# Kernel tuning notes

Measured on AMD Instinct MI355X. Metric: run time of the kernel, lower is better.

Reference implementation:

```python
import jax, jax.numpy as jnp
import numpy as np

IN_DIM = 512
HEADS = 8
HEAD_DIM = IN_DIM // HEADS
SCALE = HEAD_DIM ** -0.5


def setup_inputs() -> dict:
    key = jax.random.key(0)
    ks = jax.random.split(key, 9)
    B, C, H, W = 16, IN_DIM, 32, 32
    std = 1.0 / np.sqrt(C)  # ~ conv2d default init scale
    inp = {
        "x": jax.random.normal(ks[0], (B, C, H, W), dtype=jnp.float32),
        "wq": jax.random.normal(ks[1], (C, C), dtype=jnp.float32) * std,
        "bq": jax.random.normal(ks[2], (C,), dtype=jnp.float32) * std,
        "wk": jax.random.normal(ks[3], (C, C), dtype=jnp.float32) * std,
        "bk": jax.random.normal(ks[4], (C,), dtype=jnp.float32) * std,
        "wv": jax.random.normal(ks[5], (C, C), dtype=jnp.float32) * std,
        "bv": jax.random.normal(ks[6], (C,), dtype=jnp.float32) * std,
        "wo": jax.random.normal(ks[7], (C, C), dtype=jnp.float32) * std,
        "bo": jax.random.normal(ks[8], (C,), dtype=jnp.float32) * std,
        "gamma": jnp.zeros((1,), dtype=jnp.float32) + 0.1,  # learned residual scale
    }
    return inp


def reference(x, wq, bq, wk, bk, wv, bv, wo, bo, gamma):
    B, C, H, W = x.shape
    N = H * W
    hd = HEAD_DIM
    # flatten spatial: [B, C, N]
    xf = x.reshape(B, C, N)
    # 1x1 convs == channel matmuls: [B, C, N]
    q = jnp.einsum('oc,bcn->bon', wq, xf) + bq[None, :, None]
    k = jnp.einsum('oc,bcn->bon', wk, xf) + bk[None, :, None]
    v = jnp.einsum('oc,bcn->bon', wv, xf) + bv[None, :, None]
    # split heads: [B, heads, head_dim, N]
    q = q.reshape(B, HEADS, hd, N)
    k = k.reshape(B, HEADS, hd, N)
    v = v.reshape(B, HEADS, hd, N)
    # energy[b,h,i,j] = sum_d q[b,h,d,i] * k[b,h,d,j]
    energy = jnp.einsum('bhdi,bhdj->bhij', q, k) * SCALE
    attn = jax.nn.softmax(energy, axis=-1)  # [B, heads, N, N]
    # out[b,h,d,i] = sum_j attn[b,h,i,j] * v[b,h,d,j]
    out = jnp.einsum('bhij,bhdj->bhdi', attn, v)
    out = out.reshape(B, C, N)
    out = jnp.einsum('oc,bcn->bon', wo, out) + bo[None, :, None]
    y = gamma[0] * out.reshape(B, C, H, W) + x
    return y
```

## Files before the change

### kernel.cpp

```cpp
#include <hip/hip_runtime.h>
#include <hip/hip_bf16.h>

#define BB 16
#define CC 512
#define HH 8
#define DD 64
#define NN 1024

using f32x4  = __attribute__((ext_vector_type(4))) float;
typedef __bf16 bf16x8 __attribute__((ext_vector_type(8)));
typedef __bf16 bf16x4 __attribute__((ext_vector_type(4)));

#define MFMA16(a, b, c) __builtin_amdgcn_mfma_f32_16x16x32_bf16((a), (b), (c), 0, 0, 0)

#define WAITVM8 asm volatile("s_waitcnt vmcnt(8)" ::: "memory")
#define WAITVM4 asm volatile("s_waitcnt vmcnt(4)" ::: "memory")
#define WAITVM0 asm volatile("s_waitcnt vmcnt(0)" ::: "memory")
#define BARRIER __builtin_amdgcn_s_barrier()
#define SCHEDB  __builtin_amdgcn_sched_barrier(0)

__device__ __forceinline__ void glds16(const __hip_bfloat16* g, __hip_bfloat16* l) {
  typedef __attribute__((address_space(1))) const void gv_t;
  typedef __attribute__((address_space(3))) void lv_t;
  __builtin_amdgcn_global_load_lds((gv_t*)g, (lv_t*)l, 16, 0, 0);
}

__global__ __launch_bounds__(256) void k_prep(
    const float* __restrict__ x, __hip_bfloat16* __restrict__ xT,
    __hip_bfloat16* __restrict__ xbf,
    const float* __restrict__ wq, const float* __restrict__ wk,
    const float* __restrict__ wv, const float* __restrict__ wo,
    __hip_bfloat16* __restrict__ wqb) {
  __shared__ float tile[64][65];
  const int L = blockIdx.x;
  const int t = threadIdx.x;
  if (L >= 2048) {
    const int j = L - 2048;
    const int mat = j >> 8;
    const float* s = (mat == 0) ? wq : (mat == 1) ? wk : (mat == 2) ? wv : wo;
    __hip_bfloat16* o = wqb + (size_t)mat * CC * CC;
    const int i = ((j & 255) * 256 + t) * 4;
    float4 v = *(const float4*)(s + i);
    alignas(8) __hip_bfloat16 tm[4];
    tm[0] = __float2bfloat16(v.x);
    tm[1] = __float2bfloat16(v.y);
    tm[2] = __float2bfloat16(v.z);
    tm[3] = __float2bfloat16(v.w);
    *(bf16x4*)(o + i) = *(const bf16x4*)tm;
    return;
  }
  const int c = L & 7, r = L >> 3;
  const int b  = c * 2 + (r >> 7);
  const int rr = r & 127;
  const int bn = (rr & 15) * 64;
  const int bc = (rr >> 4) * 64;

  const float* xb = x + ((size_t)b * CC + bc) * NN + bn;
  __hip_bfloat16* xbo = xbf + ((size_t)b * CC + bc) * NN + bn;
  const int r0 = t >> 4;
  const int c0 = (t & 15) * 4;
  for (int p = 0; p < 4; ++p) {
    const int rw = r0 + p * 16;
    float4 v = *(const float4*)(xb + (size_t)rw * NN + c0);
    tile[rw][c0 + 0] = v.x;
    tile[rw][c0 + 1] = v.y;
    tile[rw][c0 + 2] = v.z;
    tile[rw][c0 + 3] = v.w;
    alignas(8) __hip_bfloat16 tm[4];
    tm[0] = __float2bfloat16(v.x);
    tm[1] = __float2bfloat16(v.y);
    tm[2] = __float2bfloat16(v.z);
    tm[3] = __float2bfloat16(v.w);
    *(bf16x4*)(xbo + (size_t)rw * NN + c0) = *(const bf16x4*)tm;
  }
  __syncthreads();

  __hip_bfloat16* xo = xT + ((size_t)b * NN + bn) * CC + bc;
  const int rn0 = t >> 3;
  const int cc0 = (t & 7) * 8;
  for (int p = 0; p < 2; ++p) {
    const int rn = rn0 + p * 32;
    alignas(16) __hip_bfloat16 tmp[8];
    for (int j = 0; j < 8; ++j) tmp[j] = __float2bfloat16(tile[cc0 + j][rn]);
    *(bf16x8*)(xo + (size_t)rn * CC + cc0) = *(const bf16x8*)tmp;
  }
}

__global__ __launch_bounds__(256, 2) void k_gemm_qkv(
    const __hip_bfloat16* __restrict__ Wqkv,
    const __hip_bfloat16* __restrict__ Xt,
    const float* __restrict__ bq, const float* __restrict__ bk,
    const float* __restrict__ bv,
    __hip_bfloat16* __restrict__ qT, __hip_bfloat16* __restrict__ kT,
    __hip_bfloat16* __restrict__ vO, float qscale) {
  __shared__ __hip_bfloat16 Wl[2][8192];
  __shared__ __hip_bfloat16 Xl[2][8192];
  const int b  = blockIdx.z;
  const int ot = blockIdx.y * 128;
  const int nt = blockIdx.x * 128;
  const int sector = blockIdx.y >> 2;
  const int t  = threadIdx.x;
  const int w  = t >> 6, l = t & 63;
  const int wr = w >> 1, wc = w & 1;
  const int lg = l >> 4, lr16 = l & 15;

  f32x4 acc[4][4] = {};

  const __hip_bfloat16* Wp = Wqkv + (size_t)ot * CC;
  const __hip_bfloat16* Xp = Xt + ((size_t)b * NN + nt) * CC;
  const int srow = w * 8 + (l >> 3);
  const int scol = ((l & 7) ^ ((l >> 3) & 7)) * 8;
  const __hip_bfloat16* wsrc = Wp + (size_t)srow * CC + scol;
  const __hip_bfloat16* xsrc = Xp + (size_t)srow * CC + scol;

  auto STAGE = [&](int bn, int k0) {
#pragma unroll
    for (int i = 0; i < 4; ++i)
      glds16(wsrc + (size_t)(i * 32) * CC + k0, &Wl[bn][(w * 8 + i * 32) * 64]);
#pragma unroll
    for (int i = 0; i < 4; ++i)
      glds16(xsrc + (size_t)(i * 32) * CC + k0, &Xl[bn][(w * 8 + i * 32) * 64]);
  };

  const int s7 = lr16 & 7;
  const int slot0 = ((lg) ^ s7) * 8;
  const int slot1 = ((4 + lg) ^ s7) * 8;
  const int rowA = (wr * 64 + lr16) * 64;
  const int rowB = (wc * 64 + lr16) * 64;

  auto STEP = [&](int bn) {
    const __hip_bfloat16* Wb = &Wl[bn][0];
    const __hip_bfloat16* Xb = &Xl[bn][0];
#pragma unroll
    for (int ks = 0; ks < 2; ++ks) {
      const int sl = ks ? slot1 : slot0;
      bf16x8 af[4], bfr[4];
#pragma unroll
      for (int mi = 0; mi < 4; ++mi) af[mi] = *(const bf16x8*)(Wb + rowA + mi * 1024 + sl);
#pragma unroll
      for (int nj = 0; nj < 4; ++nj) bfr[nj] = *(const bf16x8*)(Xb + rowB + nj * 1024 + sl);
      __builtin_amdgcn_s_setprio(1);
#pragma unroll
      for (int mi = 0; mi < 4; ++mi)
#pragma unroll
        for (int nj = 0; nj < 4; ++nj)
          acc[mi][nj] = MFMA16(af[mi], bfr[nj], acc[mi][nj]);
      __builtin_amdgcn_s_setprio(0);
    }
  };

  STAGE(0, 0);
  STAGE(1, 64);
  for (int kt = 0; kt < 7; ++kt) {
    WAITVM8;
    BARRIER; SCHEDB;
    STEP(kt & 1);
    BARRIER;
    if (kt < 6) STAGE(kt & 1, (kt + 2) * 64);
  }
  WAITVM0; BARRIER; SCHEDB; STEP(1);

  const float* bias = (sector == 0) ? bq : (sector == 1) ? bk : bv;
  const float scale = (sector == 0) ? qscale : 1.0f;
  __hip_bfloat16* outT = (sector == 0) ? qT : kT;

  for (int mi = 0; mi < 4; ++mi) {
    const int og = ot + wr * 64 + mi * 16 + lg * 4;
    const int o0 = og & 511;
    for (int nj = 0; nj < 4; ++nj) {
      const int n = nt + wc * 64 + nj * 16 + lr16;
      if (sector < 2) {
        alignas(8) __hip_bfloat16 tmp[4];
        for (int rj = 0; rj < 4; ++rj)
          tmp[rj] = __float2bfloat16((acc[mi][nj][rj] + bias[o0 + rj]) * scale);
        const int hh = o0 >> 6, d0 = o0 & 63;
        *(bf16x4*)(outT + (((size_t)(b * HH + hh)) * NN + n) * DD + d0) = *(const bf16x4*)tmp;
      } else {
        for (int rj = 0; rj < 4; ++rj)
          vO[((size_t)b * CC + o0 + rj) * NN + n] =
              __float2bfloat16(acc[mi][nj][rj] + bias[o0 + rj]);
      }
    }
  }
}

__global__ __launch_bounds__(256, 4) void k_gemm_o(
    const __hip_bfloat16* __restrict__ W,
    const __hip_bfloat16* __restrict__ Xt,
    const float* __restrict__ bias,
    const __hip_bfloat16* __restrict__ xbf,
    const float* __restrict__ gamma,
    float* __restrict__ y) {
  __shared__ __hip_bfloat16 Wl[2][4096];
  __shared__ __hip_bfloat16 Xl[2][4096];
  const int b  = blockIdx.z;
  const int ot = blockIdx.y * 128;
  const int nt = blockIdx.x * 128;
  const int t  = threadIdx.x;
  const int w  = t >> 6, l = t & 63;
  const int wr = w >> 1, wc = w & 1;
  const int lg = l >> 4, lr16 = l & 15;

  f32x4 acc[4][4] = {};

  const int srow = w * 16 + (l >> 2);
  const int scol = ((l & 3) ^ ((l >> 3) & 3)) * 8;
  const __hip_bfloat16* ws0 = W + (size_t)(ot + srow) * CC + scol;
  const __hip_bfloat16* xs0 = Xt + ((size_t)b * NN + nt + srow) * CC + scol;

  const int sx  = (lg ^ ((lr16 >> 1) & 3)) * 8;
  const int rdA = (wr * 64 + lr16) * 32 + sx;
  const int rdB = (wc * 64 + lr16) * 32 + sx;

#define STAGEO(bn, k0)                                        \
  do {                                                        \
    glds16(ws0 + (k0), &Wl[bn][w * 512]);                     \
    glds16(ws0 + (size_t)64 * CC + (k0), &Wl[bn][2048 + w * 512]); \
    glds16(xs0 + (k0), &Xl[bn][w * 512]);                     \
    glds16(xs0 + (size_t)64 * CC + (k0), &Xl[bn][2048 + w * 512]); \
  } while (0)

  STAGEO(0, 0);
  for (int kt = 0; kt < 16; ++kt) {
    WAITVM0;
    BARRIER; SCHEDB;
    if (kt < 15) STAGEO((kt + 1) & 1, (kt + 1) * 32);
    const __hip_bfloat16* Wb = &Wl[kt & 1][0];
    const __hip_bfloat16* Xb = &Xl[kt & 1][0];
    bf16x8 af[4], bfr[4];
#pragma unroll
    for (int mi = 0; mi < 4; ++mi) af[mi] = *(const bf16x8*)(Wb + rdA + mi * 512);
#pragma unroll
    for (int nj = 0; nj < 4; ++nj) bfr[nj] = *(const bf16x8*)(Xb + rdB + nj * 512);
    __builtin_amdgcn_s_setprio(1);
#pragma unroll
    for (int mi = 0; mi < 4; ++mi)
#pragma unroll
      for (int nj = 0; nj < 4; ++nj)
        acc[mi][nj] = MFMA16(af[mi], bfr[nj], acc[mi][nj]);
    __builtin_amdgcn_s_setprio(0);
  }
#undef STAGEO

  const float g = gamma[0];
  for (int mi = 0; mi < 4; ++mi) {
    const int o0 = ot + wr * 64 + mi * 16 + lg * 4;
    for (int nj = 0; nj < 4; ++nj) {
      const int n = nt + wc * 64 + nj * 16 + lr16;
      for (int rj = 0; rj < 4; ++rj) {
        const size_t idx = ((size_t)b * CC + o0 + rj) * NN + n;
        y[idx] = g * (acc[mi][nj][rj] + bias[o0 + rj]) + __bfloat162float(xbf[idx]);
      }
    }
  }
}

__global__ __launch_bounds__(256, 2) void k_attn(
    const __hip_bfloat16* __restrict__ qT,
    const __hip_bfloat16* __restrict__ kT,
    const __hip_bfloat16* __restrict__ v,
    __hip_bfloat16* __restrict__ attT) {
  __shared__ __hip_bfloat16 Kl[3][4096];
  __shared__ __hip_bfloat16 Vl[3][4096];

  const int L = blockIdx.x;
  const int c = L & 7, s = L >> 3;
  const int bh = c * 16 + (s >> 2);
  const int i0 = (s & 3) * 256;
  const int b = bh >> 3, h = bh & 7;
  const int t  = threadIdx.x;
  const int w  = t >> 6, l = t & 63;
  const int lg = l >> 4, lr = l & 15;

  const __hip_bfloat16* qb = qT + ((size_t)(b * HH + h)) * NN * DD;
  const __hip_bfloat16* kb = kT + ((size_t)(b * HH + h)) * NN * DD;
  const __hip_bfloat16* vb = v + ((size_t)b * CC + h * DD) * NN;

  bf16x8 qf[4][2];
#pragma unroll
  for (int g = 0; g < 4; ++g) {
    const __hip_bfloat16* qp = qb + (size_t)(i0 + w * 64 + g * 16 + lr) * DD + lg * 8;
    qf[g][0] = *(const bf16x8*)qp;
    qf[g][1] = *(const bf16x8*)(qp + 32);
  }

  const int rA = w * 8 + (l >> 3);
  const int rB = rA + 32;
  const int sA = (l & 7) ^ ((rA & 3) ^ (((rA >> 3) & 1) << 2));
  const __hip_bfloat16* gKA = kb + rA * DD + sA * 8;
  const __hip_bfloat16* gKB = kb + rB * DD + sA * 8;
  const __hip_bfloat16* gVA = vb + (size_t)rA * NN + sA * 8;
  const __hip_bfloat16* gVB = vb + (size_t)rB * NN + sA * 8;

  auto STAGE = [&](int bufn, int tile) {
    glds16(gKA + (size_t)tile * 4096, &Kl[bufn][w * 512]);
    glds16(gKB + (size_t)tile * 4096, &Kl[bufn][2048 + w * 512]);
    glds16(gVA + tile * 64, &Vl[bufn][w * 512]);
    glds16(gVB + tile * 64, &Vl[bufn][2048 + w * 512]);
  };

  const int swzK = (lr & 3) ^ (((lr >> 2) & 1) << 2);
  const int krl  = 8 * (lr >> 2) + (lr & 3);
  const int offK0 = krl * 64 + ((lg ^ swzK) * 8);
  const int offK1 = krl * 64 + (((lg + 4) ^ swzK) * 8);
  const int swzV = (lr & 3) ^ (((lr >> 3) & 1) << 2);

  f32x4 accO[4][4] = {};
  f32x4 accL[4] = {};
  const bf16x8 ones = {(__bf16)1.f, (__bf16)1.f, (__bf16)1.f, (__bf16)1.f,
                       (__bf16)1.f, (__bf16)1.f, (__bf16)1.f, (__bf16)1.f};

  STAGE(0, 0);
  STAGE(1, 1);
  STAGE(2, 2);

  for (int tile = 0; tile < 16; ++tile) {
    const int bufn = tile % 3;
    if (tile < 14) { WAITVM8; } else if (tile == 14) { WAITVM4; } else { WAITVM0; }
    BARRIER; SCHEDB;

    const __hip_bfloat16* Kb = &Kl[bufn][0];
    const __hip_bfloat16* Vb = &Vl[bufn][0];

    __builtin_amdgcn_s_setprio(1);
    f32x4 st[4][4];
#pragma unroll
    for (int jt = 0; jt < 4; ++jt) {
      const int jo = (jt >> 1) * 2048 + (jt & 1) * 256;
      bf16x8 kf0 = *(const bf16x8*)(Kb + jo + offK0);
      bf16x8 kf1 = *(const bf16x8*)(Kb + jo + offK1);
#pragma unroll
      for (int g = 0; g < 4; ++g) {
        f32x4 a = {};
        a = MFMA16(kf0, qf[g][0], a);
        a = MFMA16(kf1, qf[g][1], a);
        st[g][jt] = a;
      }
    }
    __builtin_amdgcn_s_setprio(0);

    bf16x8 pf[4][2];
#pragma unroll
    for (int g = 0; g < 4; ++g) {
      union { bf16x8 v8; __hip_bfloat16 h[8]; } pk0, pk1;
#pragma unroll
      for (int jt = 0; jt < 4; ++jt)
#pragma unroll
        for (int rj = 0; rj < 4; ++rj) {
          const float p = __builtin_amdgcn_exp2f(st[g][jt][rj]);
          if (jt < 2) pk0.h[(jt & 1) * 4 + rj] = __float2bfloat16(p);
          else        pk1.h[(jt & 1) * 4 + rj] = __float2bfloat16(p);
        }
      pf[g][0] = pk0.v8;
      pf[g][1] = pk1.v8;
    }

    __builtin_amdgcn_s_setprio(1);
#pragma unroll
    for (int ks = 0; ks < 2; ++ks) {
#pragma unroll
      for (int dt = 0; dt < 4; ++dt) {
        bf16x8 vf = *(const bf16x8*)(Vb + (dt * 16 + lr) * 64 + (((ks * 4 + lg) ^ swzV) * 8));
#pragma unroll
        for (int g = 0; g < 4; ++g)
          accO[g][dt] = MFMA16(pf[g][ks], vf, accO[g][dt]);
      }
#pragma unroll
      for (int g = 0; g < 4; ++g)
        accL[g] = MFMA16(pf[g][ks], ones, accL[g]);
    }
    __builtin_amdgcn_s_setprio(0);

    BARRIER;
    if (tile < 13) STAGE(bufn, tile + 3);
  }

#pragma unroll
  for (int g = 0; g < 4; ++g)
#pragma unroll
    for (int dt = 0; dt < 4; ++dt) {
      f32x4 o;
#pragma unroll
      for (int rj = 0; rj < 4; ++rj) o[rj] = accO[g][dt][rj] / accL[g][rj];
#pragma unroll
      for (int rj = 0; rj < 4; ++rj) {
        const int i = i0 + w * 64 + g * 16 + 4 * lg + rj;
        const int d = dt * 16 + lr;
        attT[((size_t)b * NN + i) * CC + h * DD + d] = __float2bfloat16(o[rj]);
      }
    }
}

extern "C" void kernel_launch(void* const* d_in, const int* in_sizes, int n_in,
                              void* d_out, int out_size, void* d_ws, size_t ws_size,
                              hipStream_t stream) {
  const float* x     = (const float*)d_in[0];
  const float* wq    = (const float*)d_in[1];
  const float* bq    = (const float*)d_in[2];
  const float* wk    = (const float*)d_in[3];
  const float* bk    = (const float*)d_in[4];
  const float* wv    = (const float*)d_in[5];
  const float* bv    = (const float*)d_in[6];
  const float* wo    = (const float*)d_in[7];
  const float* bo    = (const float*)d_in[8];
  const float* gamma = (const float*)d_in[9];
  float* y = (float*)d_out;

  char* ws = (char*)d_ws;
  const size_t szT = (size_t)BB * NN * CC * 2;
  __hip_bfloat16* xT  = (__hip_bfloat16*)(ws);
  __hip_bfloat16* qT  = (__hip_bfloat16*)(ws + szT);
  __hip_bfloat16* kTb = (__hip_bfloat16*)(ws + 2 * szT);
  __hip_bfloat16* vB  = (__hip_bfloat16*)(ws + 3 * szT);
  __hip_bfloat16* xbf = (__hip_bfloat16*)(ws + 4 * szT);
  __hip_bfloat16* wqb = (__hip_bfloat16*)(ws + 5 * szT);
  __hip_bfloat16* wob = wqb + (size_t)3 * CC * CC;

  k_prep<<<dim3(2048 + 1024), 256, 0, stream>>>(x, xT, xbf, wq, wk, wv, wo, wqb);

  const float qsc = 0.125f * 1.44269504f;
  k_gemm_qkv<<<dim3(NN / 128, 12, BB), 256, 0, stream>>>(
      wqb, xT, bq, bk, bv, qT, kTb, vB, qsc);

  k_attn<<<dim3(BB * HH * (NN / 256)), 256, 0, stream>>>(qT, kTb, vB, xT);

  k_gemm_o<<<dim3(NN / 128, CC / 128, BB), 256, 0, stream>>>(
      wob, xT, bo, xbf, gamma, y);
}
```

Baseline: 115.7 us.

## Enlarge QKV GEMM tiles to 256x256 with 8 waves and phased prefetch

The QKV projection GEMM now uses 256x256 output tiles with 512 threads (8 waves, each computing 128x64), and flattens batch and spatial into a single N dimension. The K loop is split into four phases per step that interleave the next A/B tile loads with MFMA work, double buffering A one step ahead and B two steps ahead. The goal is more data reuse per LDS load and better overlap of global-to-LDS copies with compute. The costs are 128KB of LDS per block, more accumulator registers, fewer blocks in flight, and extra barriers.

```diff
diff --git a/kernel.cpp b/kernel.cpp
--- a/kernel.cpp
+++ b/kernel.cpp
@@ -86,98 +86,123 @@
   }
 }
 
-__global__ __launch_bounds__(256, 2) void k_gemm_qkv(
+__global__ __launch_bounds__(512, 2) void k_gemm_qkv(
     const __hip_bfloat16* __restrict__ Wqkv,
     const __hip_bfloat16* __restrict__ Xt,
     const float* __restrict__ bq, const float* __restrict__ bk,
     const float* __restrict__ bv,
     __hip_bfloat16* __restrict__ qT, __hip_bfloat16* __restrict__ kT,
     __hip_bfloat16* __restrict__ vO, float qscale) {
-  __shared__ __hip_bfloat16 Wl[2][8192];
-  __shared__ __hip_bfloat16 Xl[2][8192];
-  const int b  = blockIdx.z;
-  const int ot = blockIdx.y * 128;
-  const int nt = blockIdx.x * 128;
-  const int sector = blockIdx.y >> 2;
-  const int t  = threadIdx.x;
-  const int w  = t >> 6, l = t & 63;
-  const int wr = w >> 1, wc = w & 1;
+  __shared__ __hip_bfloat16 Al[2][16384];
+  __shared__ __hip_bfloat16 Bl[2][16384];
+  const int ot = blockIdx.y * 256;
+  const int ng = blockIdx.x * 256;
+  const int sector = blockIdx.y >> 1;
+  const int t = threadIdx.x;
+  const int w = t >> 6, l = t & 63;
+  const int wr = w >> 2, wc = w & 3;
   const int lg = l >> 4, lr16 = l & 15;
 
-  f32x4 acc[4][4] = {};
+  f32x4 acc[8][4] = {};
+  bf16x8 bfr[4][2];
 
   const __hip_bfloat16* Wp = Wqkv + (size_t)ot * CC;
-  const __hip_bfloat16* Xp = Xt + ((size_t)b * NN + nt) * CC;
+  const __hip_bfloat16* Xp = Xt + (size_t)ng * CC;
   const int srow = w * 8 + (l >> 3);
   const int scol = ((l & 7) ^ ((l >> 3) & 7)) * 8;
-  const __hip_bfloat16* wsrc = Wp + (size_t)srow * CC + scol;
-  const __hip_bfloat16* xsrc = Xp + (size_t)srow * CC + scol;
-
-  auto STAGE = [&](int bn, int k0) {
-#pragma unroll
-    for (int i = 0; i < 4; ++i)
-      glds16(wsrc + (size_t)(i * 32) * CC + k0, &Wl[bn][(w * 8 + i * 32) * 64]);
-#pragma unroll
-    for (int i = 0; i < 4; ++i)
-      glds16(xsrc + (size_t)(i * 32) * CC + k0, &Xl[bn][(w * 8 + i * 32) * 64]);
+  const __hip_bfloat16* asrc = Wp + (size_t)srow * CC + scol;
+  const __hip_bfloat16* bsrc = Xp + (size_t)srow * CC + scol;
+
+  auto SA = [&](int buf, int kt, int h) {
+#pragma unroll
+    for (int i = 0; i < 2; ++i)
+      glds16(asrc + (size_t)(h * 128 + i * 64) * CC + kt * 64,
+             &Al[buf][(h * 128 + i * 64 + w * 8) * 64]);
   };
+  auto SB = [&](int buf, int kt, int h) {
+#pragma unroll
+    for (int i = 0; i < 2; ++i)
+      glds16(bsrc + (size_t)(h * 128 + i * 64) * CC + kt * 64,
+             &Bl[buf][(h * 128 + i * 64 + w * 8) * 64]);
+  };
 
   const int s7 = lr16 & 7;
-  const int slot0 = ((lg) ^ s7) * 8;
+  const int slot0 = (lg ^ s7) * 8;
   const int slot1 = ((4 + lg) ^ s7) * 8;
-  const int rowA = (wr * 64 + lr16) * 64;
+  const int rowA = (wr * 128 + lr16) * 64;
   const int rowB = (wc * 64 + lr16) * 64;
 
-  auto STEP = [&](int bn) {
-    const __hip_bfloat16* Wb = &Wl[bn][0];
-    const __hip_bfloat16* Xb = &Xl[bn][0];
-#pragma unroll
-    for (int ks = 0; ks < 2; ++ks) {
-      const int sl = ks ? slot1 : slot0;
-      bf16x8 af[4], bfr[4];
-#pragma unroll
-      for (int mi = 0; mi < 4; ++mi) af[mi] = *(const bf16x8*)(Wb + rowA + mi * 1024 + sl);
-#pragma unroll
-      for (int nj = 0; nj < 4; ++nj) bfr[nj] = *(const bf16x8*)(Xb + rowB + nj * 1024 + sl);
-      __builtin_amdgcn_s_setprio(1);
-#pragma unroll
-      for (int mi = 0; mi < 4; ++mi)
-#pragma unroll
-        for (int nj = 0; nj < 4; ++nj)
-          acc[mi][nj] = MFMA16(af[mi], bfr[nj], acc[mi][nj]);
-      __builtin_amdgcn_s_setprio(0);
-    }
-  };
-
-  STAGE(0, 0);
-  STAGE(1, 64);
-  for (int kt = 0; kt < 7; ++kt) {
-    WAITVM8;
-    BARRIER; SCHEDB;
-    STEP(kt & 1);
-    BARRIER;
-    if (kt < 6) STAGE(kt & 1, (kt + 2) * 64);
-  }
-  WAITVM0; BARRIER; SCHEDB; STEP(1);
+  SA(0, 0, 0); SA(0, 0, 1);
+  SB(0, 0, 0); SB(0, 0, 1);
+  SB(1, 1, 0); SB(1, 1, 1);
+  WAITVM4;
+  BARRIER;
+
+#define QPHASE(q, STG, WT)                                                  \
+  do {                                                                      \
+    bf16x8 a0 = *(const bf16x8*)(Ab + rowA + (2 * (q) + 0) * 1024 + slot0); \
+    bf16x8 a1 = *(const bf16x8*)(Ab + rowA + (2 * (q) + 0) * 1024 + slot1); \
+    bf16x8 a2 = *(const bf16x8*)(Ab + rowA + (2 * (q) + 1) * 1024 + slot0); \
+    bf16x8 a3 = *(const bf16x8*)(Ab + rowA + (2 * (q) + 1) * 1024 + slot1); \
+    STG;                                                                    \
+    WT;                                                                     \
+    BARRIER;                                                                \
+    asm volatile("s_waitcnt lgkmcnt(0)" ::: "memory");                      \
+    SCHEDB;                                                                 \
+    __builtin_amdgcn_s_setprio(1);                                          \
+    _Pragma("unroll")                                                       \
+    for (int nj = 0; nj < 4; ++nj) {                                        \
+      acc[2 * (q) + 0][nj] = MFMA16(a0, bfr[nj][0], acc[2 * (q) + 0][nj]);  \
+      acc[2 * (q) + 0][nj] = MFMA16(a1, bfr[nj][1], acc[2 * (q) + 0][nj]);  \
+      acc[2 * (q) + 1][nj] = MFMA16(a2, bfr[nj][0], acc[2 * (q) + 1][nj]);  \
+      acc[2 * (q) + 1][nj] = MFMA16(a3, bfr[nj][1], acc[2 * (q) + 1][nj]);  \
+    }                                                                       \
+    __builtin_amdgcn_s_setprio(0);                                          \
+    BARRIER;                                                                \
+  } while (0)
+
+  for (int j = 0; j < 8; ++j) {
+    const int p = j & 1, pn = p ^ 1;
+    const __hip_bfloat16* Ab = &Al[p][0];
+    const __hip_bfloat16* Bb = &Bl[p][0];
+#pragma unroll
+    for (int nj = 0; nj < 4; ++nj) {
+      bfr[nj][0] = *(const bf16x8*)(Bb + rowB + nj * 1024 + slot0);
+      bfr[nj][1] = *(const bf16x8*)(Bb + rowB + nj * 1024 + slot1);
+    }
+    QPHASE(0, if (j < 7) SA(pn, j + 1, 0), (void)0);
+    QPHASE(1, if (j < 7) SA(pn, j + 1, 1), (void)0);
+    QPHASE(2, if (j < 6) SB(p, j + 2, 0), (void)0);
+    QPHASE(3, if (j < 6) SB(p, j + 2, 1),
+           if (j < 6) { WAITVM4; } else { WAITVM0; });
+  }
+#undef QPHASE
 
   const float* bias = (sector == 0) ? bq : (sector == 1) ? bk : bv;
   const float scale = (sector == 0) ? qscale : 1.0f;
   __hip_bfloat16* outT = (sector == 0) ? qT : kT;
-
-  for (int mi = 0; mi < 4; ++mi) {
-    const int og = ot + wr * 64 + mi * 16 + lg * 4;
-    const int o0 = og & 511;
+  const int bb = ng >> 10;
+  const int nb = ng & 1023;
+  const int obase = (ot & 511) + wr * 128;
+
+#pragma unroll
+  for (int mi = 0; mi < 8; ++mi) {
+    const int o0 = obase + mi * 16 + lg * 4;
+#pragma unroll
     for (int nj = 0; nj < 4; ++nj) {
-      const int n = nt + wc * 64 + nj * 16 + lr16;
+      const int n = nb + wc * 64 + nj * 16 + lr16;
       if (sector < 2) {
         alignas(8) __hip_bfloat16 tmp[4];
+#pragma unroll
         for (int rj = 0; rj < 4; ++rj)
           tmp[rj] = __float2bfloat16((acc[mi][nj][rj] + bias[o0 + rj]) * scale);
         const int hh = o0 >> 6, d0 = o0 & 63;
-        *(bf16x4*)(outT + (((size_t)(b * HH + hh)) * NN + n) * DD + d0) = *(const bf16x4*)tmp;
+        *(bf16x4*)(outT + (((size_t)(bb * HH + hh)) * NN + n) * DD + d0) =
+            *(const bf16x4*)tmp;
       } else {
+#pragma unroll
         for (int rj = 0; rj < 4; ++rj)
-          vO[((size_t)b * CC + o0 + rj) * NN + n] =
+          vO[((size_t)bb * CC + o0 + rj) * NN + n] =
               __float2bfloat16(acc[mi][nj][rj] + bias[o0 + rj]);
       }
     }
@@ -419,7 +444,7 @@
   k_prep<<<dim3(2048 + 1024), 256, 0, stream>>>(x, xT, xbf, wq, wk, wv, wo, wqb);
 
   const float qsc = 0.125f * 1.44269504f;
-  k_gemm_qkv<<<dim3(NN / 128, 12, BB), 256, 0, stream>>>(
+  k_gemm_qkv<<<dim3(16384 / 256, 1536 / 256, 1), 512, 0, stream>>>(
       wqb, xT, bq, bk, bv, qT, kTb, vB, qsc);
 
   k_attn<<<dim3(BB * HH * (NN / 256)), 256, 0, stream>>>(qT, kTb, vB, xT);
```

Result: no change. 117.4 us (+1.5%).

## Widen QKV GEMM tile to 128x256 with 512 threads and triple-buffered loads

Applied to the files above, without the earlier changes.

The QKV projection GEMM now runs 512-thread blocks (8 waves in a 2x4 layout) covering 128 output channels by 256 tokens, with the batch folded into the token dimension. Shared-memory staging moves from double to triple buffering, with vmcnt waits adjusted so two tiles stay in flight. The wider tile is meant to improve reuse of the weight tile and hide global-load latency better. In exchange it uses more LDS per block (144 KB for two blocks), which may limit occupancy.

```diff
diff --git a/kernel.cpp b/kernel.cpp
--- a/kernel.cpp
+++ b/kernel.cpp
@@ -13,9 +13,11 @@
 
 #define MFMA16(a, b, c) __builtin_amdgcn_mfma_f32_16x16x32_bf16((a), (b), (c), 0, 0, 0)
 
-#define WAITVM8 asm volatile("s_waitcnt vmcnt(8)" ::: "memory")
-#define WAITVM4 asm volatile("s_waitcnt vmcnt(4)" ::: "memory")
-#define WAITVM0 asm volatile("s_waitcnt vmcnt(0)" ::: "memory")
+#define WAITVM12 asm volatile("s_waitcnt vmcnt(12)" ::: "memory")
+#define WAITVM8  asm volatile("s_waitcnt vmcnt(8)" ::: "memory")
+#define WAITVM6  asm volatile("s_waitcnt vmcnt(6)" ::: "memory")
+#define WAITVM4  asm volatile("s_waitcnt vmcnt(4)" ::: "memory")
+#define WAITVM0  asm volatile("s_waitcnt vmcnt(0)" ::: "memory")
 #define BARRIER __builtin_amdgcn_s_barrier()
 #define SCHEDB  __builtin_amdgcn_sched_barrier(0)
 
@@ -86,44 +88,43 @@
   }
 }
 
-__global__ __launch_bounds__(256, 2) void k_gemm_qkv(
+__global__ __launch_bounds__(512, 2) void k_gemm_qkv(
     const __hip_bfloat16* __restrict__ Wqkv,
     const __hip_bfloat16* __restrict__ Xt,
     const float* __restrict__ bq, const float* __restrict__ bk,
     const float* __restrict__ bv,
     __hip_bfloat16* __restrict__ qT, __hip_bfloat16* __restrict__ kT,
     __hip_bfloat16* __restrict__ vO, float qscale) {
-  __shared__ __hip_bfloat16 Wl[2][8192];
-  __shared__ __hip_bfloat16 Xl[2][8192];
-  const int b  = blockIdx.z;
+  __shared__ __hip_bfloat16 Wl[3][8192];
+  __shared__ __hip_bfloat16 Xl[3][16384];
   const int ot = blockIdx.y * 128;
-  const int nt = blockIdx.x * 128;
+  const int ng = blockIdx.x * 256;
   const int sector = blockIdx.y >> 2;
-  const int t  = threadIdx.x;
-  const int w  = t >> 6, l = t & 63;
-  const int wr = w >> 1, wc = w & 1;
+  const int t = threadIdx.x;
+  const int w = t >> 6, l = t & 63;
+  const int wr = w >> 2, wc = w & 3;
   const int lg = l >> 4, lr16 = l & 15;
 
   f32x4 acc[4][4] = {};
 
   const __hip_bfloat16* Wp = Wqkv + (size_t)ot * CC;
-  const __hip_bfloat16* Xp = Xt + ((size_t)b * NN + nt) * CC;
+  const __hip_bfloat16* Xp = Xt + (size_t)ng * CC;
   const int srow = w * 8 + (l >> 3);
   const int scol = ((l & 7) ^ ((l >> 3) & 7)) * 8;
-  const __hip_bfloat16* wsrc = Wp + (size_t)srow * CC + scol;
-  const __hip_bfloat16* xsrc = Xp + (size_t)srow * CC + scol;
-
-  auto STAGE = [&](int bn, int k0) {
+  const __hip_bfloat16* asrc = Wp + (size_t)srow * CC + scol;
+  const __hip_bfloat16* bsrc = Xp + (size_t)srow * CC + scol;
+
+  auto STAGE = [&](int buf, int kt) {
+#pragma unroll
+    for (int i = 0; i < 2; ++i)
+      glds16(asrc + (size_t)(i * 64) * CC + kt * 64, &Wl[buf][(w * 8 + i * 64) * 64]);
 #pragma unroll
     for (int i = 0; i < 4; ++i)
-      glds16(wsrc + (size_t)(i * 32) * CC + k0, &Wl[bn][(w * 8 + i * 32) * 64]);
-#pragma unroll
-    for (int i = 0; i < 4; ++i)
-      glds16(xsrc + (size_t)(i * 32) * CC + k0, &Xl[bn][(w * 8 + i * 32) * 64]);
+      glds16(bsrc + (size_t)(i * 64) * CC + kt * 64, &Xl[buf][(w * 8 + i * 64) * 64]);
   };
 
   const int s7 = lr16 & 7;
-  const int slot0 = ((lg) ^ s7) * 8;
+  const int slot0 = (lg ^ s7) * 8;
   const int slot1 = ((4 + lg) ^ s7) * 8;
   const int rowA = (wr * 64 + lr16) * 64;
   const int rowB = (wc * 64 + lr16) * 64;
@@ -150,34 +151,41 @@
   };
 
   STAGE(0, 0);
-  STAGE(1, 64);
-  for (int kt = 0; kt < 7; ++kt) {
-    WAITVM8;
+  STAGE(1, 1);
+  STAGE(2, 2);
+  for (int kt = 0; kt < 8; ++kt) {
+    if (kt < 6) { WAITVM12; } else if (kt == 6) { WAITVM6; } else { WAITVM0; }
     BARRIER; SCHEDB;
-    STEP(kt & 1);
+    STEP(kt % 3);
     BARRIER;
-    if (kt < 6) STAGE(kt & 1, (kt + 2) * 64);
-  }
-  WAITVM0; BARRIER; SCHEDB; STEP(1);
+    if (kt < 5) STAGE(kt % 3, kt + 3);
+  }
 
   const float* bias = (sector == 0) ? bq : (sector == 1) ? bk : bv;
   const float scale = (sector == 0) ? qscale : 1.0f;
   __hip_bfloat16* outT = (sector == 0) ? qT : kT;
-
+  const int bb = ng >> 10;
+  const int nb = ng & 1023;
+
+#pragma unroll
   for (int mi = 0; mi < 4; ++mi) {
     const int og = ot + wr * 64 + mi * 16 + lg * 4;
     const int o0 = og & 511;
+#pragma unroll
     for (int nj = 0; nj < 4; ++nj) {
-      const int n = nt + wc * 64 + nj * 16 + lr16;
+      const int n = nb + wc * 64 + nj * 16 + lr16;
       if (sector < 2) {
         alignas(8) __hip_bfloat16 tmp[4];
+#pragma unroll
         for (int rj = 0; rj < 4; ++rj)
           tmp[rj] = __float2bfloat16((acc[mi][nj][rj] + bias[o0 + rj]) * scale);
         const int hh = o0 >> 6, d0 = o0 & 63;
-        *(bf16x4*)(outT + (((size_t)(b * HH + hh)) * NN + n) * DD + d0) = *(const bf16x4*)tmp;
+        *(bf16x4*)(outT + (((size_t)(bb * HH + hh)) * NN + n) * DD + d0) =
+            *(const bf16x4*)tmp;
       } else {
+#pragma unroll
         for (int rj = 0; rj < 4; ++rj)
-          vO[((size_t)b * CC + o0 + rj) * NN + n] =
+          vO[((size_t)bb * CC + o0 + rj) * NN + n] =
               __float2bfloat16(acc[mi][nj][rj] + bias[o0 + rj]);
       }
     }
@@ -419,7 +427,7 @@
   k_prep<<<dim3(2048 + 1024), 256, 0, stream>>>(x, xT, xbf, wq, wk, wv, wo, wqb);
 
   const float qsc = 0.125f * 1.44269504f;
-  k_gemm_qkv<<<dim3(NN / 128, 12, BB), 256, 0, stream>>>(
+  k_gemm_qkv<<<dim3(16384 / 256, 1536 / 128, 1), 512, 0, stream>>>(
       wqb, xT, bq, bk, bv, qT, kTb, vB, qsc);
 
   k_attn<<<dim3(BB * HH * (NN / 256)), 256, 0, stream>>>(qT, kTb, vB, xT);
```

Result: no change. 117.7 us (+1.7%).

## Compute Q, K and V tiles in one persistent block to reuse the X tile

Applied to the files above, without the earlier changes.

The QKV GEMM grid shrinks from 1536 blocks to 512. Each block now walks three output sectors (Q, K, V) in sequence over a continuous 24-step pipeline, storing and zeroing its accumulators at each sector boundary. X tiles are still re-streamed per sector, so the main intent is fewer blocks, less prologue/epilogue cost, and overlap of each epilogue with the next sector's prefetch. The trade-offs are less parallelism (512 blocks on 256 CUs at 2 per CU) and an epilogue that sits inside the pipeline loop.

```diff
diff --git a/kernel.cpp b/kernel.cpp
--- a/kernel.cpp
+++ b/kernel.cpp
@@ -13,9 +13,10 @@
 
 #define MFMA16(a, b, c) __builtin_amdgcn_mfma_f32_16x16x32_bf16((a), (b), (c), 0, 0, 0)
 
-#define WAITVM8 asm volatile("s_waitcnt vmcnt(8)" ::: "memory")
-#define WAITVM4 asm volatile("s_waitcnt vmcnt(4)" ::: "memory")
-#define WAITVM0 asm volatile("s_waitcnt vmcnt(0)" ::: "memory")
+#define WAITVM16 asm volatile("s_waitcnt vmcnt(16)" ::: "memory")
+#define WAITVM8  asm volatile("s_waitcnt vmcnt(8)" ::: "memory")
+#define WAITVM4  asm volatile("s_waitcnt vmcnt(4)" ::: "memory")
+#define WAITVM0  asm volatile("s_waitcnt vmcnt(0)" ::: "memory")
 #define BARRIER __builtin_amdgcn_s_barrier()
 #define SCHEDB  __builtin_amdgcn_sched_barrier(0)
 
@@ -95,10 +96,12 @@
     __hip_bfloat16* __restrict__ vO, float qscale) {
   __shared__ __hip_bfloat16 Wl[2][8192];
   __shared__ __hip_bfloat16 Xl[2][8192];
-  const int b  = blockIdx.z;
-  const int ot = blockIdx.y * 128;
-  const int nt = blockIdx.x * 128;
-  const int sector = blockIdx.y >> 2;
+  const int bid = blockIdx.x;
+  const int by0 = bid >> 7;
+  const int bx  = bid & 127;
+  const int nt  = bx * 128;
+  const int bb  = nt >> 10;
+  const int nb  = nt & 1023;
   const int t  = threadIdx.x;
   const int w  = t >> 6, l = t & 63;
   const int wr = w >> 1, wc = w & 1;
@@ -106,17 +109,18 @@
 
   f32x4 acc[4][4] = {};
 
-  const __hip_bfloat16* Wp = Wqkv + (size_t)ot * CC;
-  const __hip_bfloat16* Xp = Xt + ((size_t)b * NN + nt) * CC;
   const int srow = w * 8 + (l >> 3);
   const int scol = ((l & 7) ^ ((l >> 3) & 7)) * 8;
-  const __hip_bfloat16* wsrc = Wp + (size_t)srow * CC + scol;
-  const __hip_bfloat16* xsrc = Xp + (size_t)srow * CC + scol;
-
-  auto STAGE = [&](int bn, int k0) {
+  const __hip_bfloat16* wsrc0 = Wqkv + (size_t)(by0 * 128 + srow) * CC + scol;
+  const __hip_bfloat16* xsrc  = Xt + ((size_t)nt + srow) * CC + scol;
+
+  auto STAGE = [&](int bn, int ktg) {
+    const int rep = ktg >> 3;
+    const int k0  = (ktg & 7) * 64;
+    const __hip_bfloat16* ws = wsrc0 + (size_t)rep * 512 * CC;
 #pragma unroll
     for (int i = 0; i < 4; ++i)
-      glds16(wsrc + (size_t)(i * 32) * CC + k0, &Wl[bn][(w * 8 + i * 32) * 64]);
+      glds16(ws + (size_t)(i * 32) * CC + k0, &Wl[bn][(w * 8 + i * 32) * 64]);
 #pragma unroll
     for (int i = 0; i < 4; ++i)
       glds16(xsrc + (size_t)(i * 32) * CC + k0, &Xl[bn][(w * 8 + i * 32) * 64]);
@@ -150,35 +154,49 @@
   };
 
   STAGE(0, 0);
-  STAGE(1, 64);
-  for (int kt = 0; kt < 7; ++kt) {
-    WAITVM8;
+  STAGE(1, 1);
+  for (int ktg = 0; ktg < 24; ++ktg) {
+    if (ktg == 23)                    { WAITVM0;  }
+    else if (ktg > 0 && (ktg & 7) == 0) { WAITVM16; }
+    else                              { WAITVM8;  }
     BARRIER; SCHEDB;
-    STEP(kt & 1);
+    STEP(ktg & 1);
     BARRIER;
-    if (kt < 6) STAGE(kt & 1, (kt + 2) * 64);
-  }
-  WAITVM0; BARRIER; SCHEDB; STEP(1);
-
-  const float* bias = (sector == 0) ? bq : (sector == 1) ? bk : bv;
-  const float scale = (sector == 0) ? qscale : 1.0f;
-  __hip_bfloat16* outT = (sector == 0) ? qT : kT;
-
-  for (int mi = 0; mi < 4; ++mi) {
-    const int og = ot + wr * 64 + mi * 16 + lg * 4;
-    const int o0 = og & 511;
-    for (int nj = 0; nj < 4; ++nj) {
-      const int n = nt + wc * 64 + nj * 16 + lr16;
-      if (sector < 2) {
-        alignas(8) __hip_bfloat16 tmp[4];
-        for (int rj = 0; rj < 4; ++rj)
-          tmp[rj] = __float2bfloat16((acc[mi][nj][rj] + bias[o0 + rj]) * scale);
-        const int hh = o0 >> 6, d0 = o0 & 63;
-        *(bf16x4*)(outT + (((size_t)(b * HH + hh)) * NN + n) * DD + d0) = *(const bf16x4*)tmp;
-      } else {
-        for (int rj = 0; rj < 4; ++rj)
-          vO[((size_t)b * CC + o0 + rj) * NN + n] =
-              __float2bfloat16(acc[mi][nj][rj] + bias[o0 + rj]);
+    if (ktg < 22) STAGE(ktg & 1, ktg + 2);
+
+    if ((ktg & 7) == 7) {
+      const int rep = ktg >> 3;
+      const float* bias = (rep == 0) ? bq : (rep == 1) ? bk : bv;
+      const float scale = (rep == 0) ? qscale : 1.0f;
+      __hip_bfloat16* outT = (rep == 0) ? qT : kT;
+#pragma unroll
+      for (int mi = 0; mi < 4; ++mi) {
+        const int o0 = by0 * 128 + wr * 64 + mi * 16 + lg * 4;
+#pragma unroll
+        for (int nj = 0; nj < 4; ++nj) {
+          const int n = nb + wc * 64 + nj * 16 + lr16;
+          if (rep < 2) {
+            alignas(8) __hip_bfloat16 tmp[4];
+#pragma unroll
+            for (int rj = 0; rj < 4; ++rj)
+              tmp[rj] = __float2bfloat16((acc[mi][nj][rj] + bias[o0 + rj]) * scale);
+            const int hh = o0 >> 6, d0 = o0 & 63;
+            *(bf16x4*)(outT + (((size_t)(bb * HH + hh)) * NN + n) * DD + d0) =
+                *(const bf16x4*)tmp;
+          } else {
+#pragma unroll
+            for (int rj = 0; rj < 4; ++rj)
+              vO[((size_t)bb * CC + o0 + rj) * NN + n] =
+                  __float2bfloat16(acc[mi][nj][rj] + bias[o0 + rj]);
+          }
+        }
+      }
+      if (ktg < 23) {
+#pragma unroll
+        for (int mi = 0; mi < 4; ++mi)
+#pragma unroll
+          for (int nj = 0; nj < 4; ++nj)
+            acc[mi][nj] = f32x4{0.f, 0.f, 0.f, 0.f};
       }
     }
   }
@@ -419,7 +437,7 @@
   k_prep<<<dim3(2048 + 1024), 256, 0, stream>>>(x, xT, xbf, wq, wk, wv, wo, wqb);
 
   const float qsc = 0.125f * 1.44269504f;
-  k_gemm_qkv<<<dim3(NN / 128, 12, BB), 256, 0, stream>>>(
+  k_gemm_qkv<<<dim3(512), 256, 0, stream>>>(
       wqb, xT, bq, bk, bv, qT, kTb, vB, qsc);
 
   k_attn<<<dim3(BB * HH * (NN / 256)), 256, 0, stream>>>(qT, kTb, vB, xT);
```

After: 112.6 us. -2.7%, faster.
